# Kernel optimization log

Hardware: AMD Instinct MI355X
Metric: run time of the kernel (lower is better)

The kernel has to match this reference:

```python
import jax, jax.numpy as jnp
import numpy as np

NUM_GRAPHS = 8192
TRAJ_LEN = 128
N = NUM_GRAPHS * TRAJ_LEN        # 1,048,576 nodes
NUM_EDGES = 8 * N                # 8,388,608 edges
DIM = 3


def setup_inputs() -> dict:
    key = jax.random.key(0)
    kP, kr, kc = jax.random.split(key, 3)
    P = jax.random.normal(kP, (N, DIM), dtype=jnp.float32)
    # sorted, contiguous graph ids: trajectories of equal length TRAJ_LEN
    B = (jnp.arange(N, dtype=jnp.int32) // TRAJ_LEN).astype(jnp.int32)
    row = jax.random.randint(kr, (NUM_EDGES,), 0, N, dtype=jnp.int32)
    col = jax.random.randint(kc, (NUM_EDGES,), 0, N, dtype=jnp.int32)
    return {"P": P, "B": B, "row": row, "col": col}


def reference(P, B, row, col):
    G = NUM_GRAPHS
    # boundary masks (B is sorted & contiguous, B[0] != B[-1])
    is_first = B != jnp.roll(B, 1)          # [N] bool
    is_last = B != jnp.roll(B, -1)          # [N] bool
    fp = is_first.astype(P.dtype)           # [N]

    ones = jnp.ones((N,), dtype=P.dtype)
    L = jax.ops.segment_sum(ones, B, num_segments=G)   # [G] trajectory lengths

    def seg_sum(x):
        return jax.ops.segment_sum(x, B, num_segments=G)

    def cumsum_per_graph(x):  # x: [N]
        cs = jnp.cumsum(x)
        mn = jax.ops.segment_min(cs, B, num_segments=G)
        fv = seg_sum(x * fp)                 # value at first point of each graph
        return cs - mn[B] + fv[B]

    def cummax_per_graph(x):  # faithful to source: cummax + first_value[B]
        cm = jax.lax.cummax(x, axis=0)
        fv = seg_sum(x * fp)
        return cm + fv[B]

    # diff_per_graph with fill_last=True
    dr = jnp.where(is_last[:, None], jnp.zeros((), P.dtype), jnp.roll(P, -1, axis=0) - P)  # [N,D]

    # scale: pos_std = sqrt(sum_d Var_d) per graph
    mean_P = seg_sum(P) / L[:, None]
    mean_P2 = seg_sum(P ** 2) / L[:, None]
    std_P = jnp.sqrt(mean_P2 - mean_P ** 2)            # [G,D]
    P_STD = jnp.sqrt(jnp.sum(std_P ** 2, axis=1))      # [G]

    # normalized time per node
    time = cumsum_per_graph(ones)                      # 1..L within each graph
    time_norm = time / L[B]                            # [N]

    node_features = [time_norm[:, None]]
    edge_features = [(time_norm[row] - time_norm[col])[:, None]]

    sf = P_STD[B][:, None]                             # [N,1]
    dr_ = dr / sf
    p = P / sf
    dr_norm = jnp.sqrt(1e-05 + jnp.sum(dr_ ** 2, axis=1))  # [N]

    cum_dist = cumsum_per_graph(dr_norm)[:, None]
    cum_msd = cumsum_per_graph(dr_norm ** 2)[:, None]
    cmx = cummax_per_graph(dr_norm)[:, None]
    node_features += [cum_dist, cum_msd, cmx]

    d = jnp.sqrt(jnp.sum((p[row] - p[col]) ** 2, axis=1))       # [E]
    corr = jnp.sum(dr_[row] * dr_[col], axis=1)                 # [E]
    edge_features += [d[:, None], corr[:, None],
                      cum_dist[row] - cum_dist[col],
                      cum_msd[row] - cum_msd[col]]

    X = jnp.concatenate(node_features, axis=1)   # [N,4]
    E = jnp.concatenate(edge_features, axis=1)   # [E,5]

    u = seg_sum(dr) / L[:, None]                               # mean jump per graph
    u = u / jnp.sqrt(1e-05 + jnp.sum(u ** 2, axis=1))[:, None]
    scales = jnp.stack([P_STD, L], axis=1)                     # [G,2]
    return X, E, scales, u
```

## Files before the change

kernel.cpp:

```cpp
#include <hip/hip_runtime.h>
#include <hip/hip_fp16.h>
#include <math.h>

#define TRAJ 128

typedef float nf4 __attribute__((ext_vector_type(4)));

static __device__ __forceinline__ unsigned int f2bf(float f) {
    unsigned int u = __float_as_uint(f);
    return (u + 0x7FFFu + ((u >> 16) & 1u)) >> 16;
}
static __device__ __forceinline__ float bf2f(unsigned int b) {
    return __uint_as_float(b << 16);
}

__global__ __launch_bounds__(TRAJ) void graph_kernel(
    const float* __restrict__ P,
    float* __restrict__ X,
    float* __restrict__ scales,
    float* __restrict__ uout,
    float* __restrict__ gmax,
    float* __restrict__ gfv,
    float* __restrict__ pack,
    int use_pack)
{
    const int g    = blockIdx.x;
    const int t    = threadIdx.x;
    const int lane = t & 63;
    const int wave = t >> 6;
    const long long i = (long long)g * TRAJ + t;

    __shared__ float sx[TRAJ + 1], sy[TRAJ + 1], sz[TRAJ + 1];
    __shared__ float sred[2][6];
    __shared__ float sw0[3];

    const float px = P[3 * i + 0];
    const float py = P[3 * i + 1];
    const float pz = P[3 * i + 2];
    sx[t] = px; sy[t] = py; sz[t] = pz;
    if (t == 0) { sx[TRAJ] = 0.0f; sy[TRAJ] = 0.0f; sz[TRAJ] = 0.0f; }

    float r0 = px, r1 = py, r2 = pz;
    float r3 = px * px, r4 = py * py, r5 = pz * pz;
    #pragma unroll
    for (int off = 32; off > 0; off >>= 1) {
        r0 += __shfl_xor(r0, off, 64);
        r1 += __shfl_xor(r1, off, 64);
        r2 += __shfl_xor(r2, off, 64);
        r3 += __shfl_xor(r3, off, 64);
        r4 += __shfl_xor(r4, off, 64);
        r5 += __shfl_xor(r5, off, 64);
    }
    if (lane == 0) {
        sred[wave][0] = r0; sred[wave][1] = r1; sred[wave][2] = r2;
        sred[wave][3] = r3; sred[wave][4] = r4; sred[wave][5] = r5;
    }
    __syncthreads();

    const float invL = 1.0f / (float)TRAJ;
    const float Sx  = sred[0][0] + sred[1][0];
    const float Sy  = sred[0][1] + sred[1][1];
    const float Sz  = sred[0][2] + sred[1][2];
    const float Sx2 = sred[0][3] + sred[1][3];
    const float Sy2 = sred[0][4] + sred[1][4];
    const float Sz2 = sred[0][5] + sred[1][5];
    const float mx = Sx * invL, my = Sy * invL, mz = Sz * invL;
    float var = (Sx2 * invL - mx * mx) + (Sy2 * invL - my * my) + (Sz2 * invL - mz * mz);
    var = fmaxf(var, 0.0f);
    const float pstd = sqrtf(var);
    const float inv  = 1.0f / pstd;

    float drx = sx[t + 1] - px;
    float dry = sy[t + 1] - py;
    float drz = sz[t + 1] - pz;
    if (t == TRAJ - 1) { drx = 0.0f; dry = 0.0f; drz = 0.0f; }
    const float dsx = drx * inv, dsy = dry * inv, dsz = drz * inv;
    const float qx  = px * inv,  qy  = py * inv,  qz  = pz * inv;
    const float dn  = sqrtf(1e-5f + dsx * dsx + dsy * dsy + dsz * dsz);
    const float dn2 = dn * dn;

    float s1 = dn, s2 = dn2, m1 = dn;
    #pragma unroll
    for (int off = 1; off < 64; off <<= 1) {
        const float a = __shfl_up(s1, (unsigned)off, 64);
        const float b = __shfl_up(s2, (unsigned)off, 64);
        const float c = __shfl_up(m1, (unsigned)off, 64);
        if (lane >= off) { s1 += a; s2 += b; m1 = fmaxf(m1, c); }
    }
    if (t == 63) { sw0[0] = s1; sw0[1] = s2; sw0[2] = m1; }
    __syncthreads();
    if (wave == 1) {
        s1 += sw0[0];
        s2 += sw0[1];
        m1 = fmaxf(m1, sw0[2]);
    }

    if (t == 0) {
        gfv[g] = dn;
        scales[2 * g + 0] = pstd;
        scales[2 * g + 1] = (float)TRAJ;
        float ux = (sx[TRAJ - 1] - sx[0]) * invL;
        float uy = (sy[TRAJ - 1] - sy[0]) * invL;
        float uz = (sz[TRAJ - 1] - sz[0]) * invL;
        const float un = 1.0f / sqrtf(1e-5f + ux * ux + uy * uy + uz * uz);
        uout[3 * g + 0] = ux * un;
        uout[3 * g + 1] = uy * un;
        uout[3 * g + 2] = uz * un;
    }
    if (t == TRAJ - 1) gmax[g] = m1;

    const float tn = (float)(t + 1) * invL;
    {
        nf4 xr = { tn, s1, s2, m1 };
        __builtin_nontemporal_store(xr, (nf4*)X + i);
    }

    if (use_pack) {
        unsigned int w0 = f2bf(qx)  | (f2bf(qy)  << 16);
        unsigned int w1 = f2bf(qz)  | (f2bf(dsx) << 16);
        unsigned int w2 = f2bf(dsy) | (f2bf(dsz) << 16);
        unsigned int w3 = (unsigned int)__half_as_ushort(__float2half(s1))
                        | ((unsigned int)__half_as_ushort(__float2half(s2)) << 16);
        nf4 pk = { __uint_as_float(w0), __uint_as_float(w1),
                   __uint_as_float(w2), __uint_as_float(w3) };
        __builtin_nontemporal_store(pk, (nf4*)pack + i);
    }
}

__global__ __launch_bounds__(1024) void scanmax_kernel(
    const float* __restrict__ gmax, float* __restrict__ pgm, int G)
{
    const int t = threadIdx.x;
    const int lane = t & 63;
    const int wv = t >> 6;
    const int CH = (G + 1023) >> 10;

    float loc[16];
    float run = 0.0f;
    for (int k = 0; k < CH; ++k) {
        const int g = t * CH + k;
        const float v = (g < G) ? gmax[g] : 0.0f;
        loc[k] = run;
        run = fmaxf(run, v);
    }
    float inc = run;
    #pragma unroll
    for (int off = 1; off < 64; off <<= 1) {
        const float a = __shfl_up(inc, (unsigned)off, 64);
        if (lane >= off) inc = fmaxf(inc, a);
    }
    __shared__ float swt[16];
    if (lane == 63) swt[wv] = inc;
    __syncthreads();
    float excl = __shfl_up(inc, 1u, 64);
    if (lane == 0) excl = 0.0f;
    for (int w = 0; w < wv; ++w) excl = fmaxf(excl, swt[w]);

    for (int k = 0; k < CH; ++k) {
        const int g = t * CH + k;
        if (g < G) pgm[g] = fmaxf(excl, loc[k]);
    }
}

__global__ __launch_bounds__(256) void fixup_kernel(
    float* __restrict__ X, const float* __restrict__ pgm,
    const float* __restrict__ gfv, int N)
{
    const int i = blockIdx.x * 256 + threadIdx.x;
    if (i >= N) return;
    const int g = i >> 7;
    const long long idx = 4ll * i + 3;
    const float v = __builtin_nontemporal_load(&X[idx]);
    __builtin_nontemporal_store(fmaxf(pgm[g], v) + gfv[g], &X[idx]);
}

__global__ __launch_bounds__(256) void edge_kernel(
    const int* __restrict__ row, const int* __restrict__ col,
    const float4* __restrict__ pack, float* __restrict__ Eout, int E)
{
    __shared__ float sm[256 * 5];
    const int t = threadIdx.x;
    const long long e = (long long)blockIdx.x * 256 + t;

    float f0 = 0.f, f1 = 0.f, f2 = 0.f, f3 = 0.f, f4 = 0.f;
    if (e < E) {
        const int r = __builtin_nontemporal_load(&row[e]);
        const int c = __builtin_nontemporal_load(&col[e]);
        const float4 pr = pack[r];
        const float4 pc = pack[c];

        const unsigned int r0 = __float_as_uint(pr.x);
        const unsigned int r1 = __float_as_uint(pr.y);
        const unsigned int r2 = __float_as_uint(pr.z);
        const unsigned int r3 = __float_as_uint(pr.w);
        const unsigned int c0 = __float_as_uint(pc.x);
        const unsigned int c1 = __float_as_uint(pc.y);
        const unsigned int c2 = __float_as_uint(pc.z);
        const unsigned int c3 = __float_as_uint(pc.w);

        const float rpx = bf2f(r0 & 0xFFFFu), rpy = bf2f(r0 >> 16);
        const float rpz = bf2f(r1 & 0xFFFFu), rdx = bf2f(r1 >> 16);
        const float rdy = bf2f(r2 & 0xFFFFu), rdz = bf2f(r2 >> 16);
        const float cpx = bf2f(c0 & 0xFFFFu), cpy = bf2f(c0 >> 16);
        const float cpz = bf2f(c1 & 0xFFFFu), cdx = bf2f(c1 >> 16);
        const float cdy = bf2f(c2 & 0xFFFFu), cdz = bf2f(c2 >> 16);
        const float rcd = __half2float(__ushort_as_half((unsigned short)(r3 & 0xFFFFu)));
        const float rcm = __half2float(__ushort_as_half((unsigned short)(r3 >> 16)));
        const float ccd = __half2float(__ushort_as_half((unsigned short)(c3 & 0xFFFFu)));
        const float ccm = __half2float(__ushort_as_half((unsigned short)(c3 >> 16)));

        f0 = (float)((r & (TRAJ - 1)) - (c & (TRAJ - 1))) * (1.0f / (float)TRAJ);
        const float dx = rpx - cpx, dy = rpy - cpy, dz = rpz - cpz;
        f1 = sqrtf(dx * dx + dy * dy + dz * dz);
        f2 = rdx * cdx + rdy * cdy + rdz * cdz;
        f3 = rcd - ccd;
        f4 = rcm - ccm;
    }
    sm[t * 5 + 0] = f0;
    sm[t * 5 + 1] = f1;
    sm[t * 5 + 2] = f2;
    sm[t * 5 + 3] = f3;
    sm[t * 5 + 4] = f4;
    __syncthreads();
    const long long bb = (long long)blockIdx.x * (256 * 5);
    const long long lim = 5ll * E;
    #pragma unroll
    for (int k = 0; k < 5; ++k) {
        const long long gi = bb + k * 256 + t;
        if (gi < lim) __builtin_nontemporal_store(sm[k * 256 + t], &Eout[gi]);
    }
}

__global__ __launch_bounds__(256) void edge_kernel_nopack(
    const int* __restrict__ row, const int* __restrict__ col,
    const float* __restrict__ X, const float* __restrict__ P,
    const float* __restrict__ scales, float* __restrict__ Eout, int E)
{
    __shared__ float sm[256 * 5];
    const int t = threadIdx.x;
    const long long e = (long long)blockIdx.x * 256 + t;

    float f0 = 0.f, f1 = 0.f, f2 = 0.f, f3 = 0.f, f4 = 0.f;
    if (e < E) {
        const int r = row[e], c = col[e];
        const float4* X4 = (const float4*)X;
        const float4 xr = X4[r], xc = X4[c];
        const float ir = 1.0f / scales[2 * (r >> 7)];
        const float ic = 1.0f / scales[2 * (c >> 7)];
        const float prx = P[3ll * r], pry = P[3ll * r + 1], prz = P[3ll * r + 2];
        const float pcx = P[3ll * c], pcy = P[3ll * c + 1], pcz = P[3ll * c + 2];
        float drx = 0.f, dry = 0.f, drz = 0.f;
        if ((r & (TRAJ - 1)) != TRAJ - 1) {
            drx = (P[3ll * r + 3] - prx) * ir;
            dry = (P[3ll * r + 4] - pry) * ir;
            drz = (P[3ll * r + 5] - prz) * ir;
        }
        float dcx = 0.f, dcy = 0.f, dcz = 0.f;
        if ((c & (TRAJ - 1)) != TRAJ - 1) {
            dcx = (P[3ll * c + 3] - pcx) * ic;
            dcy = (P[3ll * c + 4] - pcy) * ic;
            dcz = (P[3ll * c + 5] - pcz) * ic;
        }
        const float dx = prx * ir - pcx * ic;
        const float dy = pry * ir - pcy * ic;
        const float dz = prz * ir - pcz * ic;
        f0 = (float)((r & (TRAJ - 1)) - (c & (TRAJ - 1))) * (1.0f / (float)TRAJ);
        f1 = sqrtf(dx * dx + dy * dy + dz * dz);
        f2 = drx * dcx + dry * dcy + drz * dcz;
        f3 = xr.y - xc.y;
        f4 = xr.z - xc.z;
    }
    sm[t * 5 + 0] = f0;
    sm[t * 5 + 1] = f1;
    sm[t * 5 + 2] = f2;
    sm[t * 5 + 3] = f3;
    sm[t * 5 + 4] = f4;
    __syncthreads();
    const long long bb = (long long)blockIdx.x * (256 * 5);
    const long long lim = 5ll * E;
    #pragma unroll
    for (int k = 0; k < 5; ++k) {
        const long long gi = bb + k * 256 + t;
        if (gi < lim) Eout[gi] = sm[k * 256 + t];
    }
}

extern "C" void kernel_launch(void* const* d_in, const int* in_sizes, int n_in,
                              void* d_out, int out_size, void* d_ws, size_t ws_size,
                              hipStream_t stream) {
    const float* P  = (const float*)d_in[0];
    const int* row  = (const int*)d_in[2];
    const int* col  = (const int*)d_in[3];

    const int N = in_sizes[1];
    const int E = in_sizes[2];
    const int G = N / TRAJ;

    float* X      = (float*)d_out;
    float* Eout   = X + (size_t)N * 4;
    float* scales = Eout + (size_t)E * 5;
    float* uout   = scales + (size_t)G * 2;

    float* gmax = (float*)d_ws;
    float* gfv  = gmax + G;
    float* pgm  = gfv + G;
    size_t packoff = ((size_t)(3 * G) * sizeof(float) + 15) & ~(size_t)15;
    float* pack = (float*)((char*)d_ws + packoff);
    const size_t need = packoff + (size_t)N * sizeof(float4);
    const int use_pack = (ws_size >= need) ? 1 : 0;

    graph_kernel<<<G, TRAJ, 0, stream>>>(P, X, scales, uout, gmax, gfv, pack, use_pack);
    scanmax_kernel<<<1, 1024, 0, stream>>>(gmax, pgm, G);
    fixup_kernel<<<(N + 255) / 256, 256, 0, stream>>>(X, pgm, gfv, N);
    if (use_pack) {
        edge_kernel<<<(E + 255) / 256, 256, 0, stream>>>(row, col, (const float4*)pack, Eout, E);
    } else {
        edge_kernel_nopack<<<(E + 255) / 256, 256, 0, stream>>>(row, col, X, P, scales, Eout, E);
    }
}
```

Measured before the change: 474.5 us.

## Fuse cummax fixup into edge kernel and process four edges per thread

Folds the per-node cummax fixup pass into the edge kernel, where the first 128 threads of each block grid-stride over nodes, which removes one kernel launch. Each thread now handles four edges and issues all row/col and pack gathers before computing, so more memory requests are in flight. The X and pack writes in the graph kernel switch from nontemporal to regular stores so they are more likely to stay in cache for the later fixup and gathers. Shared memory per block grows fourfold, which may lower occupancy.

```diff
diff --git a/kernel.cpp b/kernel.cpp
--- a/kernel.cpp
+++ b/kernel.cpp
@@ -3,6 +3,7 @@
 #include <math.h>
 
 #define TRAJ 128
+#define EPT 4
 
 typedef float nf4 __attribute__((ext_vector_type(4)));
 
@@ -112,7 +113,7 @@
     const float tn = (float)(t + 1) * invL;
     {
         nf4 xr = { tn, s1, s2, m1 };
-        __builtin_nontemporal_store(xr, (nf4*)X + i);
+        ((nf4*)X)[i] = xr;
     }
 
     if (use_pack) {
@@ -123,7 +124,7 @@
                         | ((unsigned int)__half_as_ushort(__float2half(s2)) << 16);
         nf4 pk = { __uint_as_float(w0), __uint_as_float(w1),
                    __uint_as_float(w2), __uint_as_float(w3) };
-        __builtin_nontemporal_store(pk, (nf4*)pack + i);
+        ((nf4*)pack)[i] = pk;
     }
 }
 
@@ -176,27 +177,50 @@
 
 __global__ __launch_bounds__(256) void edge_kernel(
     const int* __restrict__ row, const int* __restrict__ col,
-    const float4* __restrict__ pack, float* __restrict__ Eout, int E)
-{
-    __shared__ float sm[256 * 5];
+    const float4* __restrict__ pack, float* __restrict__ Eout, int E,
+    float* __restrict__ X, const float* __restrict__ pgm,
+    const float* __restrict__ gfv, int N)
+{
+    __shared__ float sm[256 * EPT * 5];
     const int t = threadIdx.x;
-    const long long e = (long long)blockIdx.x * 256 + t;
-
-    float f0 = 0.f, f1 = 0.f, f2 = 0.f, f3 = 0.f, f4 = 0.f;
-    if (e < E) {
-        const int r = __builtin_nontemporal_load(&row[e]);
-        const int c = __builtin_nontemporal_load(&col[e]);
-        const float4 pr = pack[r];
-        const float4 pc = pack[c];
-
-        const unsigned int r0 = __float_as_uint(pr.x);
-        const unsigned int r1 = __float_as_uint(pr.y);
-        const unsigned int r2 = __float_as_uint(pr.z);
-        const unsigned int r3 = __float_as_uint(pr.w);
-        const unsigned int c0 = __float_as_uint(pc.x);
-        const unsigned int c1 = __float_as_uint(pc.y);
-        const unsigned int c2 = __float_as_uint(pc.z);
-        const unsigned int c3 = __float_as_uint(pc.w);
+    const long long base = (long long)blockIdx.x * (256 * EPT);
+
+    if (t < TRAJ) {
+        for (long long nb = (long long)blockIdx.x * TRAJ + t; nb < (long long)N;
+             nb += (long long)gridDim.x * TRAJ) {
+            const int g = (int)(nb >> 7);
+            const long long idx = 4ll * nb + 3;
+            const float v = X[idx];
+            __builtin_nontemporal_store(fmaxf(pgm[g], v) + gfv[g], &X[idx]);
+        }
+    }
+
+    int r[EPT], c[EPT];
+    #pragma unroll
+    for (int k = 0; k < EPT; ++k) {
+        const long long e = base + (long long)k * 256 + t;
+        const bool ok = e < (long long)E;
+        r[k] = ok ? __builtin_nontemporal_load(&row[e]) : 0;
+        c[k] = ok ? __builtin_nontemporal_load(&col[e]) : 0;
+    }
+
+    float4 pr[EPT], pc[EPT];
+    #pragma unroll
+    for (int k = 0; k < EPT; ++k) {
+        pr[k] = pack[r[k]];
+        pc[k] = pack[c[k]];
+    }
+
+    #pragma unroll
+    for (int k = 0; k < EPT; ++k) {
+        const unsigned int r0 = __float_as_uint(pr[k].x);
+        const unsigned int r1 = __float_as_uint(pr[k].y);
+        const unsigned int r2 = __float_as_uint(pr[k].z);
+        const unsigned int r3 = __float_as_uint(pr[k].w);
+        const unsigned int c0 = __float_as_uint(pc[k].x);
+        const unsigned int c1 = __float_as_uint(pc[k].y);
+        const unsigned int c2 = __float_as_uint(pc[k].z);
+        const unsigned int c3 = __float_as_uint(pc[k].w);
 
         const float rpx = bf2f(r0 & 0xFFFFu), rpy = bf2f(r0 >> 16);
         const float rpz = bf2f(r1 & 0xFFFFu), rdx = bf2f(r1 >> 16);
@@ -209,25 +233,28 @@
         const float ccd = __half2float(__ushort_as_half((unsigned short)(c3 & 0xFFFFu)));
         const float ccm = __half2float(__ushort_as_half((unsigned short)(c3 >> 16)));
 
-        f0 = (float)((r & (TRAJ - 1)) - (c & (TRAJ - 1))) * (1.0f / (float)TRAJ);
+        const float f0 = (float)((r[k] & (TRAJ - 1)) - (c[k] & (TRAJ - 1))) * (1.0f / (float)TRAJ);
         const float dx = rpx - cpx, dy = rpy - cpy, dz = rpz - cpz;
-        f1 = sqrtf(dx * dx + dy * dy + dz * dz);
-        f2 = rdx * cdx + rdy * cdy + rdz * cdz;
-        f3 = rcd - ccd;
-        f4 = rcm - ccm;
-    }
-    sm[t * 5 + 0] = f0;
-    sm[t * 5 + 1] = f1;
-    sm[t * 5 + 2] = f2;
-    sm[t * 5 + 3] = f3;
-    sm[t * 5 + 4] = f4;
-    __syncthreads();
-    const long long bb = (long long)blockIdx.x * (256 * 5);
+        const float f1 = sqrtf(dx * dx + dy * dy + dz * dz);
+        const float f2 = rdx * cdx + rdy * cdy + rdz * cdz;
+        const float f3 = rcd - ccd;
+        const float f4 = rcm - ccm;
+
+        const int el = k * 256 + t;
+        sm[el * 5 + 0] = f0;
+        sm[el * 5 + 1] = f1;
+        sm[el * 5 + 2] = f2;
+        sm[el * 5 + 3] = f3;
+        sm[el * 5 + 4] = f4;
+    }
+    __syncthreads();
+
+    const long long bb = base * 5;
     const long long lim = 5ll * E;
     #pragma unroll
-    for (int k = 0; k < 5; ++k) {
-        const long long gi = bb + k * 256 + t;
-        if (gi < lim) __builtin_nontemporal_store(sm[k * 256 + t], &Eout[gi]);
+    for (int j = 0; j < 5 * EPT; ++j) {
+        const long long gi = bb + (long long)j * 256 + t;
+        if (gi < lim) __builtin_nontemporal_store(sm[j * 256 + t], &Eout[gi]);
     }
 }
 
@@ -311,10 +338,12 @@
 
     graph_kernel<<<G, TRAJ, 0, stream>>>(P, X, scales, uout, gmax, gfv, pack, use_pack);
     scanmax_kernel<<<1, 1024, 0, stream>>>(gmax, pgm, G);
-    fixup_kernel<<<(N + 255) / 256, 256, 0, stream>>>(X, pgm, gfv, N);
     if (use_pack) {
-        edge_kernel<<<(E + 255) / 256, 256, 0, stream>>>(row, col, (const float4*)pack, Eout, E);
+        const int eb = (E + 256 * EPT - 1) / (256 * EPT);
+        edge_kernel<<<eb, 256, 0, stream>>>(row, col, (const float4*)pack, Eout, E,
+                                            X, pgm, gfv, N);
     } else {
+        fixup_kernel<<<(N + 255) / 256, 256, 0, stream>>>(X, pgm, gfv, N);
         edge_kernel_nopack<<<(E + 255) / 256, 256, 0, stream>>>(row, col, X, P, scales, Eout, E);
     }
 }
```

New measurement: 478.7 us. Within noise of the previous version (+0.9%).
